# Performance work log

Measured on AMD Instinct MI355X. Metric: run time of the kernel, lower is better.

The kernel has to match this reference:

```python
import jax, jax.numpy as jnp
import numpy as np


def setup_inputs() -> dict:
    key = jax.random.key(0)
    k1, k2 = jax.random.split(key)
    b, t, d = 4, 2048, 1024
    x = jax.random.normal(k1, (b, t, d), dtype=jnp.float32)
    # torch Linear weight has shape [out_features, in_features] = [3*d, d]
    W_qkv = jax.random.normal(k2, (3 * d, d), dtype=jnp.float32) * (2.0 / (d + 3 * d)) ** 0.5
    return {"x": x, "W_qkv": W_qkv}


def reference(x, W_qkv):
    b, t, d = x.shape
    scale = d ** -0.5
    qkv = jnp.einsum('btd,ed->bte', x, W_qkv)          # [b, t, 3d]
    # rearrange 'b t (d k) -> k b t d' with k=3: last axis splits as (d, 3)
    qkv = qkv.reshape(b, t, d, 3)
    q, k, v = qkv[..., 0], qkv[..., 1], qkv[..., 2]     # each [b, t, d]
    scores = jnp.einsum('bid,bjd->bij', q, k) * scale   # [b, t, t]
    attn = jax.nn.softmax(scores, axis=-1)
    return jnp.einsum('bij,bjd->bid', attn, v)          # [b, t, d]
```

## Files before the change

### kernel.cpp

```cpp
#include <hip/hip_runtime.h>
#include <math.h>

#define NBATCH 4
#define TDIM 2048
#define DDIM 1024

typedef __attribute__((ext_vector_type(8))) short short8;
typedef __attribute__((ext_vector_type(4))) float floatx4;
typedef __attribute__((ext_vector_type(4))) unsigned short ushort4v;

__device__ __forceinline__ unsigned short f2bf(float f) {
  unsigned int u = __float_as_uint(f);
  u += 0x7fffu + ((u >> 16) & 1u);
  return (unsigned short)(u >> 16);
}

__device__ __forceinline__ void gload_lds16(const ushort* g, ushort* l) {
  __builtin_amdgcn_global_load_lds(
      (const __attribute__((address_space(1))) void*)g,
      (__attribute__((address_space(3))) void*)l, 16, 0, 0);
}

__device__ __forceinline__ void mfma_gemm_core(
    const ushort* __restrict__ Abase, const ushort* __restrict__ Bbase,
    int lda, int ldb, int K, ushort* As, ushort* Bs, floatx4 acc[4][4]) {
  const int tid = threadIdx.x;
  const int wave = tid >> 6;
  const int lane = tid & 63;
  const int l15 = lane & 15;
  const int quad = lane >> 4;
  const int wm = wave >> 1, wn = wave & 1;

  const int srow = wave * 32 + (lane >> 3);
  const int schunk = (lane & 7) ^ ((lane >> 3) & 7);
  const ushort* ag = Abase + (size_t)srow * lda + schunk * 8;
  const ushort* bg = Bbase + (size_t)srow * ldb + schunk * 8;
  ushort* al = As + wave * 32 * 64;
  ushort* bl = Bs + wave * 32 * 64;

  const int slot = quad ^ (l15 & 7);
  const int abase = (wm * 64 + l15) * 64 + slot * 8;
  const int bbase = (wn * 64 + l15) * 64 + slot * 8;

  for (int kt = 0; kt < K; kt += 64) {
#pragma unroll
    for (int i = 0; i < 4; ++i) {
      gload_lds16(ag + kt + (size_t)(8 * i) * lda, al + 8 * i * 64);
      gload_lds16(bg + kt + (size_t)(8 * i) * ldb, bl + 8 * i * 64);
    }
    __syncthreads();
#pragma unroll
    for (int g = 0; g < 2; ++g) {
      const int ab = abase ^ (g * 32);
      const int bb = bbase ^ (g * 32);
      short8 af[4], bfr[4];
#pragma unroll
      for (int t = 0; t < 4; ++t) {
        af[t] = *(const short8*)&As[ab + t * 1024];
        bfr[t] = *(const short8*)&Bs[bb + t * 1024];
      }
#pragma unroll
      for (int i = 0; i < 4; ++i)
#pragma unroll
        for (int j = 0; j < 4; ++j)
          acc[i][j] =
              __builtin_amdgcn_mfma_f32_16x16x32_bf16(af[i], bfr[j], acc[i][j], 0, 0, 0);
    }
    __syncthreads();
  }
}

__device__ __forceinline__ void stage_B_half(const ushort* B, int ldb, int kt,
                                             ushort* Bs, int h, int w, int lane) {
#pragma unroll
  for (int i = 0; i < 2; ++i) {
    const int rb = h * 128 + w * 16 + 8 * i;
    const int r = rb + (lane >> 3);
    const int c = (lane & 7) ^ ((lane >> 3) & 7);
    gload_lds16(B + (size_t)r * ldb + kt + c * 8, Bs + rb * 64);
  }
}

__device__ __forceinline__ void stage_A_half(const ushort* A, int lda, int kt,
                                             ushort* As, int mh, int w, int lane) {
#pragma unroll
  for (int i = 0; i < 2; ++i) {
    const int g = w * 2 + i;
    const int rb = mh * 64 + (g & 7) * 8 + (g >> 3) * 128;
    const int r = rb + (lane >> 3);
    const int c = (lane & 7) ^ ((lane >> 3) & 7);
    gload_lds16(A + (size_t)r * lda + kt + c * 8, As + rb * 64);
  }
}

__device__ __forceinline__ void mfma_core256(
    const ushort* __restrict__ A, const ushort* __restrict__ B, int lda,
    int ldb, int K, ushort* As0, ushort* As1, ushort* Bs0, ushort* Bs1,
    floatx4 acc[8][4]) {
  const int tid = threadIdx.x;
  const int w = tid >> 6, lane = tid & 63;
  const int l15 = lane & 15, quad = lane >> 4;
  const int wm = w >> 2, wn = w & 3;
  const int slot = (quad ^ (l15 & 7)) * 8;
  const int abase = (wm * 128 + l15) * 64 + slot;
  const int bbase = (wn * 64 + l15) * 64 + slot;
  const int NT = K >> 6;

  stage_B_half(B, ldb, 0, Bs0, 0, w, lane);
  stage_B_half(B, ldb, 0, Bs0, 1, w, lane);
  stage_A_half(A, lda, 0, As0, 0, w, lane);
  stage_A_half(A, lda, 0, As0, 1, w, lane);
  asm volatile("s_waitcnt vmcnt(2)" ::: "memory");
  __builtin_amdgcn_s_barrier();

  const ushort* cA = As0;
  const ushort* cB = Bs0;
  ushort* nA = As1;
  ushort* nB = Bs1;

#pragma unroll 1
  for (int t = 0; t < NT; ++t) {
    const int ktn = (t + 1) << 6;
    const bool pf = (t + 1 < NT);
    short8 bf0[2][2], bf1[2][2], af[4][2];

#pragma unroll
    for (int f = 0; f < 2; ++f)
#pragma unroll
      for (int g = 0; g < 2; ++g)
        bf0[f][g] = *(const short8*)&cB[(bbase + f * 1024) ^ (g * 32)];
#pragma unroll
    for (int f = 0; f < 4; ++f)
#pragma unroll
      for (int g = 0; g < 2; ++g)
        af[f][g] = *(const short8*)&cA[(abase + f * 1024) ^ (g * 32)];
    if (pf) stage_B_half(B, ldb, ktn, nB, 0, w, lane);
    __builtin_amdgcn_s_barrier();
    __builtin_amdgcn_s_setprio(1);
#pragma unroll
    for (int f = 0; f < 4; ++f)
#pragma unroll
      for (int fj = 0; fj < 2; ++fj)
#pragma unroll
        for (int g = 0; g < 2; ++g)
          acc[f][fj] = __builtin_amdgcn_mfma_f32_16x16x32_bf16(
              af[f][g], bf0[fj][g], acc[f][fj], 0, 0, 0);
    __builtin_amdgcn_s_setprio(0);
    __builtin_amdgcn_s_barrier();

#pragma unroll
    for (int f = 0; f < 2; ++f)
#pragma unroll
      for (int g = 0; g < 2; ++g)
        bf1[f][g] = *(const short8*)&cB[(bbase + 2048 + f * 1024) ^ (g * 32)];
    if (pf) stage_B_half(B, ldb, ktn, nB, 1, w, lane);
    __builtin_amdgcn_s_barrier();
    __builtin_amdgcn_s_setprio(1);
#pragma unroll
    for (int f = 0; f < 4; ++f)
#pragma unroll
      for (int fj = 0; fj < 2; ++fj)
#pragma unroll
        for (int g = 0; g < 2; ++g)
          acc[f][2 + fj] = __builtin_amdgcn_mfma_f32_16x16x32_bf16(
              af[f][g], bf1[fj][g], acc[f][2 + fj], 0, 0, 0);
    __builtin_amdgcn_s_setprio(0);
    if (pf) asm volatile("s_waitcnt vmcnt(4)" ::: "memory");
    else    asm volatile("s_waitcnt vmcnt(0)" ::: "memory");
    __builtin_amdgcn_s_barrier();

#pragma unroll
    for (int f = 0; f < 4; ++f)
#pragma unroll
      for (int g = 0; g < 2; ++g)
        af[f][g] = *(const short8*)&cA[(abase + 4096 + f * 1024) ^ (g * 32)];
    if (pf) stage_A_half(A, lda, ktn, nA, 0, w, lane);
    __builtin_amdgcn_s_barrier();
    __builtin_amdgcn_s_setprio(1);
#pragma unroll
    for (int f = 0; f < 4; ++f)
#pragma unroll
      for (int fj = 0; fj < 2; ++fj)
#pragma unroll
        for (int g = 0; g < 2; ++g)
          acc[4 + f][fj] = __builtin_amdgcn_mfma_f32_16x16x32_bf16(
              af[f][g], bf0[fj][g], acc[4 + f][fj], 0, 0, 0);
    __builtin_amdgcn_s_setprio(0);
    __builtin_amdgcn_s_barrier();

    if (pf) stage_A_half(A, lda, ktn, nA, 1, w, lane);
    __builtin_amdgcn_s_barrier();
    __builtin_amdgcn_s_setprio(1);
#pragma unroll
    for (int f = 0; f < 4; ++f)
#pragma unroll
      for (int fj = 0; fj < 2; ++fj)
#pragma unroll
        for (int g = 0; g < 2; ++g)
          acc[4 + f][2 + fj] = __builtin_amdgcn_mfma_f32_16x16x32_bf16(
              af[f][g], bf1[fj][g], acc[4 + f][2 + fj], 0, 0, 0);
    __builtin_amdgcn_s_setprio(0);
    if (pf) asm volatile("s_waitcnt vmcnt(2)" ::: "memory");
    __builtin_amdgcn_s_barrier();

    ushort* tmp = nA; nA = (ushort*)cA; cA = tmp;
    tmp = nB; nB = (ushort*)cB; cB = tmp;
  }
}

__global__ __launch_bounds__(256) void convert_xw(
    const float* __restrict__ x, const float* __restrict__ W,
    ushort* __restrict__ xb, ushort* __restrict__ wb) {
  const int bid = blockIdx.x;
  if (bid < 8192) {
    const size_t i = (size_t)bid * 256 + threadIdx.x;
    float4 v = reinterpret_cast<const float4*>(x)[i];
    ushort4v h = {f2bf(v.x), f2bf(v.y), f2bf(v.z), f2bf(v.w)};
    reinterpret_cast<ushort4v*>(xb)[i] = h;
  } else {
    const int e = bid - 8192;
    const int c = e % 3, ii = e / 3;
    const float scale = (c == 0) ? 0.03125f : 1.0f;
    const float4 v = reinterpret_cast<const float4*>(W + (size_t)e * DDIM)[threadIdx.x];
    ushort4v h = {f2bf(v.x * scale), f2bf(v.y * scale), f2bf(v.z * scale),
                  f2bf(v.w * scale)};
    reinterpret_cast<ushort4v*>(wb + (size_t)(c * DDIM + ii) * DDIM)[threadIdx.x] = h;
  }
}

__global__ __launch_bounds__(512, 2) void qkv_gemm8(
    const ushort* __restrict__ xb, const ushort* __restrict__ wb,
    ushort* __restrict__ qb, ushort* __restrict__ kb, ushort* __restrict__ vt) {
  __shared__ __align__(16) ushort As0[256 * 64], As1[256 * 64];
  __shared__ __align__(16) ushort Bs0[256 * 64], Bs1[256 * 64];
  const int m0 = blockIdx.y * 256;
  const int n0 = blockIdx.x * 256;
  floatx4 acc[8][4];
  const floatx4 z4 = {0.f, 0.f, 0.f, 0.f};
#pragma unroll
  for (int i = 0; i < 8; ++i)
#pragma unroll
    for (int j = 0; j < 4; ++j) acc[i][j] = z4;

  mfma_core256(xb + (size_t)m0 * DDIM, wb + (size_t)n0 * DDIM, DDIM, DDIM,
               DDIM, As0, As1, Bs0, Bs1, acc);

  const int tid = threadIdx.x;
  const int w = tid >> 6, lane = tid & 63;
  const int l15 = lane & 15, quad = lane >> 4;
  const int wm = w >> 2, wn = w & 3;

  if (n0 < 2 * DDIM) {
    ushort* dst = (n0 < DDIM) ? qb : kb;
    const int cb = (n0 < DDIM) ? n0 : n0 - DDIM;
#pragma unroll
    for (int i = 0; i < 8; ++i) {
      const int rbase = m0 + wm * 128 + i * 16 + quad * 4;
#pragma unroll
      for (int j = 0; j < 4; ++j) {
        const int col = cb + wn * 64 + j * 16 + l15;
#pragma unroll
        for (int r = 0; r < 4; ++r)
          dst[(size_t)(rbase + r) * DDIM + col] = f2bf(acc[i][j][r]);
      }
    }
  } else {
#pragma unroll
    for (int i = 0; i < 8; ++i) {
      const int row = m0 + wm * 128 + i * 16 + quad * 4;
      const int b = row >> 11, t = row & (TDIM - 1);
#pragma unroll
      for (int j = 0; j < 4; ++j) {
        const int d = (n0 - 2 * DDIM) + wn * 64 + j * 16 + l15;
        ushort4v pk = {f2bf(acc[i][j][0]), f2bf(acc[i][j][1]),
                       f2bf(acc[i][j][2]), f2bf(acc[i][j][3])};
        *reinterpret_cast<ushort4v*>(&vt[(size_t)((b << 10) + d) * TDIM + t]) = pk;
      }
    }
  }
}

__global__ __launch_bounds__(512, 2) void score_gemm8(
    const ushort* __restrict__ qb, const ushort* __restrict__ kb,
    ushort* __restrict__ Sb, float* __restrict__ lpart) {
  __shared__ __align__(16) ushort As0[256 * 64], As1[256 * 64];
  __shared__ __align__(16) ushort Bs0[256 * 64], Bs1[256 * 64];
  const int z = blockIdx.z;
  const int m0 = blockIdx.y * 256;
  const int n0 = blockIdx.x * 256;
  floatx4 acc[8][4];
  const floatx4 z4 = {0.f, 0.f, 0.f, 0.f};
#pragma unroll
  for (int i = 0; i < 8; ++i)
#pragma unroll
    for (int j = 0; j < 4; ++j) acc[i][j] = z4;

  mfma_core256(qb + ((size_t)z * TDIM + m0) * DDIM,
               kb + ((size_t)z * TDIM + n0) * DDIM, DDIM, DDIM, DDIM, As0, As1,
               Bs0, Bs1, acc);

  const int tid = threadIdx.x;
  const int w = tid >> 6, lane = tid & 63;
  const int l15 = lane & 15, quad = lane >> 4;
  const int wm = w >> 2, wn = w & 3;

  ushort* S = Sb + (size_t)z * TDIM * TDIM;
#pragma unroll
  for (int i = 0; i < 8; ++i)
#pragma unroll
    for (int j = 0; j < 4; ++j)
#pragma unroll
      for (int r = 0; r < 4; ++r) acc[i][j][r] = __expf(acc[i][j][r]);

#pragma unroll
  for (int i = 0; i < 8; ++i) {
    const int rbase = m0 + wm * 128 + i * 16 + quad * 4;
#pragma unroll
    for (int j = 0; j < 4; ++j) {
      const int col = n0 + wn * 64 + j * 16 + l15;
#pragma unroll
      for (int r = 0; r < 4; ++r)
        S[(size_t)(rbase + r) * TDIM + col] = f2bf(acc[i][j][r]);
    }
  }

  float* sums = reinterpret_cast<float*>(As0);
  __syncthreads();
#pragma unroll
  for (int i = 0; i < 8; ++i) {
#pragma unroll
    for (int r = 0; r < 4; ++r) {
      float s = acc[i][0][r] + acc[i][1][r] + acc[i][2][r] + acc[i][3][r];
#pragma unroll
      for (int off = 8; off > 0; off >>= 1) s += __shfl_down(s, off, 16);
      if (l15 == 0) sums[(wm * 128 + i * 16 + quad * 4 + r) * 4 + wn] = s;
    }
  }
  __syncthreads();
  if (tid < 256)
    lpart[((size_t)z * 8 + blockIdx.x) * TDIM + m0 + tid] =
        sums[tid * 4] + sums[tid * 4 + 1] + sums[tid * 4 + 2] + sums[tid * 4 + 3];
}

__global__ __launch_bounds__(256, 3) void pv_gemm(
    const ushort* __restrict__ Pb, const ushort* __restrict__ vt,
    const float* __restrict__ lpart, float* __restrict__ out) {
  __shared__ __align__(16) ushort As[128 * 64];
  __shared__ __align__(16) ushort Bs[128 * 64];
  const int z = blockIdx.z;
  const int m0 = blockIdx.y * 128;
  const int n0 = blockIdx.x * 128;
  floatx4 acc[4][4];
  const floatx4 z4 = {0.f, 0.f, 0.f, 0.f};
#pragma unroll
  for (int i = 0; i < 4; ++i)
#pragma unroll
    for (int j = 0; j < 4; ++j) acc[i][j] = z4;

  mfma_gemm_core(Pb + (size_t)z * TDIM * TDIM + (size_t)m0 * TDIM,
                 vt + (size_t)z * DDIM * TDIM + (size_t)n0 * TDIM, TDIM, TDIM,
                 TDIM, As, Bs, acc);

  const int tid = threadIdx.x;
  const int wave = tid >> 6, lane = tid & 63;
  const int l15 = lane & 15, quad = lane >> 4;
  const int wm = wave >> 1, wn = wave & 1;

  float* linv = reinterpret_cast<float*>(As);
  __syncthreads();
  if (tid < 128) {
    float s = 0.f;
#pragma unroll
    for (int nb = 0; nb < 8; ++nb)
      s += lpart[((size_t)z * 8 + nb) * TDIM + m0 + tid];
    linv[tid] = 1.0f / s;
  }
  __syncthreads();

  float* O = out + (size_t)z * TDIM * DDIM;
#pragma unroll
  for (int i = 0; i < 4; ++i) {
    const int rl = wm * 64 + i * 16 + quad * 4;
    const int rbase = m0 + rl;
#pragma unroll
    for (int j = 0; j < 4; ++j) {
      const int col = n0 + wn * 64 + j * 16 + l15;
#pragma unroll
      for (int r = 0; r < 4; ++r)
        O[(size_t)(rbase + r) * DDIM + col] = acc[i][j][r] * linv[rl + r];
    }
  }
}

extern "C" void kernel_launch(void* const* d_in, const int* in_sizes, int n_in,
                              void* d_out, int out_size, void* d_ws, size_t ws_size,
                              hipStream_t stream) {
  const float* x = (const float*)d_in[0];
  const float* W = (const float*)d_in[1];
  float* out = (float*)d_out;

  ushort* ws = (ushort*)d_ws;
  const size_t n_x = (size_t)NBATCH * TDIM * DDIM;
  const size_t n_w = (size_t)3 * DDIM * DDIM;
  ushort* xb = ws;
  ushort* wb = xb + n_x;
  ushort* qb = wb + n_w;
  ushort* kb = qb + n_x;
  ushort* vt = kb + n_x;
  ushort* Sb = vt + n_x;
  float* lpart = (float*)(Sb + (size_t)NBATCH * TDIM * TDIM);

  convert_xw<<<dim3(8192 + 3 * DDIM), 256, 0, stream>>>(x, W, xb, wb);
  qkv_gemm8<<<dim3(3 * DDIM / 256, NBATCH * TDIM / 256), 512, 0, stream>>>(
      xb, wb, qb, kb, vt);
  score_gemm8<<<dim3(TDIM / 256, TDIM / 256, NBATCH), 512, 0, stream>>>(
      qb, kb, Sb, lpart);
  pv_gemm<<<dim3(DDIM / 128, TDIM / 128, NBATCH), 256, 0, stream>>>(Sb, vt,
                                                                    lpart, out);
}
```

Before: 240.7 us.

## Restructure 256-tile GEMM pipeline with fewer barriers and XCD-aware block swizzle

Rewrites the 256x256 MFMA main loop so each phase issues the next tile's global-to-LDS loads right after its fragment reads. It drops half the barriers, peels the last iteration so no per-iteration prefetch predicate is needed, and reorders the B staging layout to match the new phase order. All three GEMM kernels also switch to 1D grids with an XCD-aware swizzle, so blocks sharing operands land on the same chiplet L2. The added risk is that the tighter vmcnt/barrier accounting could let LDS reuse race.

```diff
diff --git a/kernel.cpp b/kernel.cpp
--- a/kernel.cpp
+++ b/kernel.cpp
@@ -19,6 +19,10 @@
   __builtin_amdgcn_global_load_lds(
       (const __attribute__((address_space(1))) void*)g,
       (__attribute__((address_space(3))) void*)l, 16, 0, 0);
+}
+
+__device__ __forceinline__ int xcd_swz(int lin, int nwg) {
+  return (lin & 7) * (nwg >> 3) + (lin >> 3);
 }
 
 __device__ __forceinline__ void mfma_gemm_core(
@@ -70,17 +74,6 @@
   }
 }
 
-__device__ __forceinline__ void stage_B_half(const ushort* B, int ldb, int kt,
-                                             ushort* Bs, int h, int w, int lane) {
-#pragma unroll
-  for (int i = 0; i < 2; ++i) {
-    const int rb = h * 128 + w * 16 + 8 * i;
-    const int r = rb + (lane >> 3);
-    const int c = (lane & 7) ^ ((lane >> 3) & 7);
-    gload_lds16(B + (size_t)r * ldb + kt + c * 8, Bs + rb * 64);
-  }
-}
-
 __device__ __forceinline__ void stage_A_half(const ushort* A, int lda, int kt,
                                              ushort* As, int mh, int w, int lane) {
 #pragma unroll
@@ -93,7 +86,19 @@
   }
 }
 
-__device__ __forceinline__ void mfma_core256(
+__device__ __forceinline__ void stage_B_half(const ushort* B, int ldb, int kt,
+                                             ushort* Bs, int nh, int w, int lane) {
+#pragma unroll
+  for (int i = 0; i < 2; ++i) {
+    const int g = w * 2 + i;
+    const int rb = (g >> 2) * 64 + nh * 32 + (g & 3) * 8;
+    const int r = rb + (lane >> 3);
+    const int c = (lane & 7) ^ ((lane >> 3) & 7);
+    gload_lds16(B + (size_t)r * ldb + kt + c * 8, Bs + rb * 64);
+  }
+}
+
+__device__ __forceinline__ void mfma_core256d3(
     const ushort* __restrict__ A, const ushort* __restrict__ B, int lda,
     int ldb, int K, ushort* As0, ushort* As1, ushort* Bs0, ushort* Bs1,
     floatx4 acc[8][4]) {
@@ -106,36 +111,33 @@
   const int bbase = (wn * 64 + l15) * 64 + slot;
   const int NT = K >> 6;
 
+  stage_A_half(A, lda, 0, As0, 0, w, lane);
   stage_B_half(B, ldb, 0, Bs0, 0, w, lane);
   stage_B_half(B, ldb, 0, Bs0, 1, w, lane);
-  stage_A_half(A, lda, 0, As0, 0, w, lane);
   stage_A_half(A, lda, 0, As0, 1, w, lane);
-  asm volatile("s_waitcnt vmcnt(2)" ::: "memory");
-  __builtin_amdgcn_s_barrier();
 
   const ushort* cA = As0;
   const ushort* cB = Bs0;
   ushort* nA = As1;
   ushort* nB = Bs1;
+  short8 af[4][2], bf0[2][2], bf1[2][2];
 
 #pragma unroll 1
-  for (int t = 0; t < NT; ++t) {
+  for (int t = 0; t < NT - 1; ++t) {
     const int ktn = (t + 1) << 6;
-    const bool pf = (t + 1 < NT);
-    short8 bf0[2][2], bf1[2][2], af[4][2];
-
+    asm volatile("s_waitcnt vmcnt(4)" ::: "memory");
+    __builtin_amdgcn_s_barrier();
+#pragma unroll
+    for (int f = 0; f < 4; ++f)
+#pragma unroll
+      for (int g = 0; g < 2; ++g)
+        af[f][g] = *(const short8*)&cA[(abase + f * 1024) ^ (g * 32)];
 #pragma unroll
     for (int f = 0; f < 2; ++f)
 #pragma unroll
       for (int g = 0; g < 2; ++g)
         bf0[f][g] = *(const short8*)&cB[(bbase + f * 1024) ^ (g * 32)];
-#pragma unroll
-    for (int f = 0; f < 4; ++f)
-#pragma unroll
-      for (int g = 0; g < 2; ++g)
-        af[f][g] = *(const short8*)&cA[(abase + f * 1024) ^ (g * 32)];
-    if (pf) stage_B_half(B, ldb, ktn, nB, 0, w, lane);
-    __builtin_amdgcn_s_barrier();
+    stage_A_half(A, lda, ktn, nA, 0, w, lane);
     __builtin_amdgcn_s_setprio(1);
 #pragma unroll
     for (int f = 0; f < 4; ++f)
@@ -146,15 +148,14 @@
           acc[f][fj] = __builtin_amdgcn_mfma_f32_16x16x32_bf16(
               af[f][g], bf0[fj][g], acc[f][fj], 0, 0, 0);
     __builtin_amdgcn_s_setprio(0);
+    asm volatile("s_waitcnt vmcnt(4)" ::: "memory");
     __builtin_amdgcn_s_barrier();
-
 #pragma unroll
     for (int f = 0; f < 2; ++f)
 #pragma unroll
       for (int g = 0; g < 2; ++g)
         bf1[f][g] = *(const short8*)&cB[(bbase + 2048 + f * 1024) ^ (g * 32)];
-    if (pf) stage_B_half(B, ldb, ktn, nB, 1, w, lane);
-    __builtin_amdgcn_s_barrier();
+    stage_B_half(B, ldb, ktn, nB, 0, w, lane);
     __builtin_amdgcn_s_setprio(1);
 #pragma unroll
     for (int f = 0; f < 4; ++f)
@@ -165,17 +166,14 @@
           acc[f][2 + fj] = __builtin_amdgcn_mfma_f32_16x16x32_bf16(
               af[f][g], bf1[fj][g], acc[f][2 + fj], 0, 0, 0);
     __builtin_amdgcn_s_setprio(0);
-    if (pf) asm volatile("s_waitcnt vmcnt(4)" ::: "memory");
-    else    asm volatile("s_waitcnt vmcnt(0)" ::: "memory");
+    asm volatile("s_waitcnt vmcnt(4)" ::: "memory");
     __builtin_amdgcn_s_barrier();
-
 #pragma unroll
     for (int f = 0; f < 4; ++f)
 #pragma unroll
       for (int g = 0; g < 2; ++g)
         af[f][g] = *(const short8*)&cA[(abase + 4096 + f * 1024) ^ (g * 32)];
-    if (pf) stage_A_half(A, lda, ktn, nA, 0, w, lane);
-    __builtin_amdgcn_s_barrier();
+    stage_B_half(B, ldb, ktn, nB, 1, w, lane);
     __builtin_amdgcn_s_setprio(1);
 #pragma unroll
     for (int f = 0; f < 4; ++f)
@@ -186,10 +184,7 @@
           acc[4 + f][fj] = __builtin_amdgcn_mfma_f32_16x16x32_bf16(
               af[f][g], bf0[fj][g], acc[4 + f][fj], 0, 0, 0);
     __builtin_amdgcn_s_setprio(0);
-    __builtin_amdgcn_s_barrier();
-
-    if (pf) stage_A_half(A, lda, ktn, nA, 1, w, lane);
-    __builtin_amdgcn_s_barrier();
+    stage_A_half(A, lda, ktn, nA, 1, w, lane);
     __builtin_amdgcn_s_setprio(1);
 #pragma unroll
     for (int f = 0; f < 4; ++f)
@@ -200,12 +195,75 @@
           acc[4 + f][2 + fj] = __builtin_amdgcn_mfma_f32_16x16x32_bf16(
               af[f][g], bf1[fj][g], acc[4 + f][2 + fj], 0, 0, 0);
     __builtin_amdgcn_s_setprio(0);
-    if (pf) asm volatile("s_waitcnt vmcnt(2)" ::: "memory");
-    __builtin_amdgcn_s_barrier();
 
     ushort* tmp = nA; nA = (ushort*)cA; cA = tmp;
     tmp = nB; nB = (ushort*)cB; cB = tmp;
   }
+
+  asm volatile("s_waitcnt vmcnt(4)" ::: "memory");
+  __builtin_amdgcn_s_barrier();
+#pragma unroll
+  for (int f = 0; f < 4; ++f)
+#pragma unroll
+    for (int g = 0; g < 2; ++g)
+      af[f][g] = *(const short8*)&cA[(abase + f * 1024) ^ (g * 32)];
+#pragma unroll
+  for (int f = 0; f < 2; ++f)
+#pragma unroll
+    for (int g = 0; g < 2; ++g)
+      bf0[f][g] = *(const short8*)&cB[(bbase + f * 1024) ^ (g * 32)];
+  __builtin_amdgcn_s_setprio(1);
+#pragma unroll
+  for (int f = 0; f < 4; ++f)
+#pragma unroll
+    for (int fj = 0; fj < 2; ++fj)
+#pragma unroll
+      for (int g = 0; g < 2; ++g)
+        acc[f][fj] = __builtin_amdgcn_mfma_f32_16x16x32_bf16(
+            af[f][g], bf0[fj][g], acc[f][fj], 0, 0, 0);
+  __builtin_amdgcn_s_setprio(0);
+  asm volatile("s_waitcnt vmcnt(2)" ::: "memory");
+  __builtin_amdgcn_s_barrier();
+#pragma unroll
+  for (int f = 0; f < 2; ++f)
+#pragma unroll
+    for (int g = 0; g < 2; ++g)
+      bf1[f][g] = *(const short8*)&cB[(bbase + 2048 + f * 1024) ^ (g * 32)];
+  __builtin_amdgcn_s_setprio(1);
+#pragma unroll
+  for (int f = 0; f < 4; ++f)
+#pragma unroll
+    for (int fj = 0; fj < 2; ++fj)
+#pragma unroll
+      for (int g = 0; g < 2; ++g)
+        acc[f][2 + fj] = __builtin_amdgcn_mfma_f32_16x16x32_bf16(
+            af[f][g], bf1[fj][g], acc[f][2 + fj], 0, 0, 0);
+  __builtin_amdgcn_s_setprio(0);
+  asm volatile("s_waitcnt vmcnt(0)" ::: "memory");
+  __builtin_amdgcn_s_barrier();
+#pragma unroll
+  for (int f = 0; f < 4; ++f)
+#pragma unroll
+    for (int g = 0; g < 2; ++g)
+      af[f][g] = *(const short8*)&cA[(abase + 4096 + f * 1024) ^ (g * 32)];
+  __builtin_amdgcn_s_setprio(1);
+#pragma unroll
+  for (int f = 0; f < 4; ++f)
+#pragma unroll
+    for (int fj = 0; fj < 2; ++fj)
+#pragma unroll
+      for (int g = 0; g < 2; ++g)
+        acc[4 + f][fj] = __builtin_amdgcn_mfma_f32_16x16x32_bf16(
+            af[f][g], bf0[fj][g], acc[4 + f][fj], 0, 0, 0);
+#pragma unroll
+  for (int f = 0; f < 4; ++f)
+#pragma unroll
+    for (int fj = 0; fj < 2; ++fj)
+#pragma unroll
+      for (int g = 0; g < 2; ++g)
+        acc[4 + f][2 + fj] = __builtin_amdgcn_mfma_f32_16x16x32_bf16(
+            af[f][g], bf1[fj][g], acc[4 + f][2 + fj], 0, 0, 0);
+  __builtin_amdgcn_s_setprio(0);
 }
 
 __global__ __launch_bounds__(256) void convert_xw(
@@ -233,8 +291,10 @@
     ushort* __restrict__ qb, ushort* __restrict__ kb, ushort* __restrict__ vt) {
   __shared__ __align__(16) ushort As0[256 * 64], As1[256 * 64];
   __shared__ __align__(16) ushort Bs0[256 * 64], Bs1[256 * 64];
-  const int m0 = blockIdx.y * 256;
-  const int n0 = blockIdx.x * 256;
+  const int swz = xcd_swz(blockIdx.x, 384);
+  const int bx = swz % 12, by = swz / 12;
+  const int m0 = by * 256;
+  const int n0 = bx * 256;
   floatx4 acc[8][4];
   const floatx4 z4 = {0.f, 0.f, 0.f, 0.f};
 #pragma unroll
@@ -242,8 +302,8 @@
 #pragma unroll
     for (int j = 0; j < 4; ++j) acc[i][j] = z4;
 
-  mfma_core256(xb + (size_t)m0 * DDIM, wb + (size_t)n0 * DDIM, DDIM, DDIM,
-               DDIM, As0, As1, Bs0, Bs1, acc);
+  mfma_core256d3(xb + (size_t)m0 * DDIM, wb + (size_t)n0 * DDIM, DDIM, DDIM,
+                 DDIM, As0, As1, Bs0, Bs1, acc);
 
   const int tid = threadIdx.x;
   const int w = tid >> 6, lane = tid & 63;
@@ -285,9 +345,10 @@
     ushort* __restrict__ Sb, float* __restrict__ lpart) {
   __shared__ __align__(16) ushort As0[256 * 64], As1[256 * 64];
   __shared__ __align__(16) ushort Bs0[256 * 64], Bs1[256 * 64];
-  const int z = blockIdx.z;
-  const int m0 = blockIdx.y * 256;
-  const int n0 = blockIdx.x * 256;
+  const int swz = xcd_swz(blockIdx.x, 256);
+  const int bx = swz & 7, by = (swz >> 3) & 7, z = swz >> 6;
+  const int m0 = by * 256;
+  const int n0 = bx * 256;
   floatx4 acc[8][4];
   const floatx4 z4 = {0.f, 0.f, 0.f, 0.f};
 #pragma unroll
@@ -295,9 +356,9 @@
 #pragma unroll
     for (int j = 0; j < 4; ++j) acc[i][j] = z4;
 
-  mfma_core256(qb + ((size_t)z * TDIM + m0) * DDIM,
-               kb + ((size_t)z * TDIM + n0) * DDIM, DDIM, DDIM, DDIM, As0, As1,
-               Bs0, Bs1, acc);
+  mfma_core256d3(qb + ((size_t)z * TDIM + m0) * DDIM,
+                 kb + ((size_t)z * TDIM + n0) * DDIM, DDIM, DDIM, DDIM, As0,
+                 As1, Bs0, Bs1, acc);
 
   const int tid = threadIdx.x;
   const int w = tid >> 6, lane = tid & 63;
@@ -338,7 +399,7 @@
   }
   __syncthreads();
   if (tid < 256)
-    lpart[((size_t)z * 8 + blockIdx.x) * TDIM + m0 + tid] =
+    lpart[((size_t)z * 8 + bx) * TDIM + m0 + tid] =
         sums[tid * 4] + sums[tid * 4 + 1] + sums[tid * 4 + 2] + sums[tid * 4 + 3];
 }
 
@@ -347,9 +408,10 @@
     const float* __restrict__ lpart, float* __restrict__ out) {
   __shared__ __align__(16) ushort As[128 * 64];
   __shared__ __align__(16) ushort Bs[128 * 64];
-  const int z = blockIdx.z;
-  const int m0 = blockIdx.y * 128;
-  const int n0 = blockIdx.x * 128;
+  const int swz = xcd_swz(blockIdx.x, 512);
+  const int bx = swz & 7, by = (swz >> 3) & 15, z = swz >> 7;
+  const int m0 = by * 128;
+  const int n0 = bx * 128;
   floatx4 acc[4][4];
   const floatx4 z4 = {0.f, 0.f, 0.f, 0.f};
 #pragma unroll
@@ -411,10 +473,7 @@
   float* lpart = (float*)(Sb + (size_t)NBATCH * TDIM * TDIM);
 
   convert_xw<<<dim3(8192 + 3 * DDIM), 256, 0, stream>>>(x, W, xb, wb);
-  qkv_gemm8<<<dim3(3 * DDIM / 256, NBATCH * TDIM / 256), 512, 0, stream>>>(
-      xb, wb, qb, kb, vt);
-  score_gemm8<<<dim3(TDIM / 256, TDIM / 256, NBATCH), 512, 0, stream>>>(
-      qb, kb, Sb, lpart);
-  pv_gemm<<<dim3(DDIM / 128, TDIM / 128, NBATCH), 256, 0, stream>>>(Sb, vt,
-                                                                    lpart, out);
-}
+  qkv_gemm8<<<dim3(384), 512, 0, stream>>>(xb, wb, qb, kb, vt);
+  score_gemm8<<<dim3(256), 512, 0, stream>>>(qb, kb, Sb, lpart);
+  pv_gemm<<<dim3(512), 256, 0, stream>>>(Sb, vt, lpart, out);
+}
```

New measurement: 218.1 us. -9.4%, faster.
